# Kernel tuning notes

Measured on AMD Instinct MI355X. Metric: run time of the kernel, lower is better.

Reference implementation:

```python
import jax, jax.numpy as jnp
import numpy as np

BN_EPS = 1e-5
N_SH, N_SS, N_HH, D = 1195, 390, 805, 64


def _gcn(x, edge_index, W, b, n_nodes, mean):
    # per-edge message = Linear(x_j); lin(x)[src] == lin(x[src])
    h = x @ W + b                                   # [N, out]
    msg = h[edge_index[0]]                          # gather sources -> [E, out]
    agg = jax.ops.segment_sum(msg, edge_index[1], num_segments=n_nodes)
    if mean:
        cnt = jax.ops.segment_sum(jnp.ones((edge_index.shape[1],), x.dtype),
                                  edge_index[1], num_segments=n_nodes)
        agg = agg / jnp.maximum(cnt, 1.0)[:, None]
    return jnp.tanh(agg)


def _bn(x, gamma, beta):
    # BatchNorm1d in training mode: biased batch statistics
    m = jnp.mean(x, axis=0)
    v = jnp.var(x, axis=0)
    return (x - m) * jax.lax.rsqrt(v + BN_EPS) * gamma + beta


def setup_inputs() -> dict:
    key = jax.random.key(0)
    ks = jax.random.split(key, 40)
    f32 = jnp.float32

    def lin(k, din, dout):
        k1, k2 = jax.random.split(k)
        s = 1.0 / np.sqrt(din)
        W = jax.random.uniform(k1, (din, dout), f32, -s, s)
        b = jax.random.uniform(k2, (dout,), f32, -s, s)
        return W, b

    inp = {}
    inp["x_SH"] = jnp.arange(N_SH, dtype=jnp.int64 if jax.config.jax_enable_x64 else jnp.int32)
    inp["edge_index_SH"] = jax.random.randint(ks[0], (2, 1_000_000), 0, N_SH)
    inp["x_SS"] = jnp.arange(N_SS)
    inp["edge_index_SS"] = jax.random.randint(ks[1], (2, 200_000), 0, N_SS)
    inp["x_HH"] = jnp.arange(N_HH)
    inp["edge_index_HH"] = jax.random.randint(ks[2], (2, 200_000), 0, N_HH)
    inp["prescription"] = jax.random.uniform(ks[3], (20000, N_SS), f32)
    inp["kgOneHot"] = jax.random.uniform(ks[4], (N_HH, 27), f32)

    inp["emb"] = jax.random.normal(ks[5], (N_SH, D), f32)
    inp["w_sh1"], inp["b_sh1"] = lin(ks[6], D, D)
    inp["w_sh2"], inp["b_sh2"] = lin(ks[7], D, D)
    inp["w_mlp1"], inp["b_mlp1"] = lin(ks[8], D, 256)
    inp["g_bn1"] = jnp.ones((256,), f32); inp["be_bn1"] = jnp.zeros((256,), f32)
    inp["w_sh1h"], inp["b_sh1h"] = lin(ks[9], D, D)
    inp["w_sh2h"], inp["b_sh2h"] = lin(ks[10], D, D)
    inp["w_mlp1h"], inp["b_mlp1h"] = lin(ks[11], D, 256)
    inp["g_bn1h"] = jnp.ones((256,), f32); inp["be_bn1h"] = jnp.zeros((256,), f32)
    inp["w_ss"], inp["b_ss"] = lin(ks[12], D, 256)
    inp["w_hh"], inp["b_hh"] = lin(ks[13], D + 27, 256)
    inp["w_mlp"], inp["b_mlp"] = lin(ks[14], 256, 256)
    inp["g_si"] = jnp.ones((256,), f32); inp["be_si"] = jnp.zeros((256,), f32)
    return inp


def reference(x_SH, edge_index_SH, x_SS, edge_index_SS, x_HH, edge_index_HH,
              prescription, kgOneHot, emb,
              w_sh1, b_sh1, w_sh2, b_sh2, w_mlp1, b_mlp1, g_bn1, be_bn1,
              w_sh1h, b_sh1h, w_sh2h, b_sh2h, w_mlp1h, b_mlp1h, g_bn1h, be_bn1h,
              w_ss, b_ss, w_hh, b_hh, w_mlp, b_mlp, g_si, be_si):
    # symptom branch on SH graph (mean aggregation)
    x1 = emb[x_SH]                                           # [1195, 64]
    x2 = _gcn(x1, edge_index_SH, w_sh1, b_sh1, N_SH, mean=True)
    x6 = _gcn(x2, edge_index_SH, w_sh2, b_sh2, N_SH, mean=True)
    x9 = (x1 + x2 + x6) / 3.0
    x9 = jnp.tanh(_bn(x9 @ w_mlp1 + b_mlp1, g_bn1, be_bn1))  # [1195, 256]

    # herb branch on SH graph
    x22 = _gcn(x1, edge_index_SH, w_sh1h, b_sh1h, N_SH, mean=True)
    x66 = _gcn(x22, edge_index_SH, w_sh2h, b_sh2h, N_SH, mean=True)
    x99 = (x1 + x22 + x66) / 3.0
    x99 = jnp.tanh(_bn(x99 @ w_mlp1h + b_mlp1h, g_bn1h, be_bn1h))

    # SS graph (add aggregation)
    x_ss1 = _gcn(emb[x_SS], edge_index_SS, w_ss, b_ss, N_SS, mean=False)  # [390, 256]

    # HH graph with KG one-hot features appended
    x_hh0 = jnp.concatenate([emb[x_HH], kgOneHot], axis=-1)  # [805, 91]
    x_hh1 = _gcn(x_hh0, edge_index_HH, w_hh, b_hh, N_HH, mean=False)      # [805, 256]

    es = x9[:N_SS] + x_ss1                                   # [390, 256]
    eh = x99[N_SS:] + x_hh1                                  # [805, 256]

    e_synd = prescription @ es                               # [B, 256]
    pre_sum = jnp.sum(prescription, axis=1, keepdims=True)
    e = e_synd / pre_sum
    e = jax.nn.relu(_bn(e @ w_mlp + b_mlp, g_si, be_si))
    return e @ eh.T                                          # [B, 805]
```

## Files before the change

kernel.cpp:

```cpp
#include <hip/hip_runtime.h>
#include <cstddef>
#include <cstdint>

#define N_SH 1195
#define N_SS 390
#define N_HH 805
#define DIM  64

typedef __bf16 bf16_t;
typedef bf16_t bf16x4v __attribute__((ext_vector_type(4)));
typedef bf16_t bf16x8v __attribute__((ext_vector_type(8)));
typedef float f32x4 __attribute__((ext_vector_type(4)));

__device__ inline ushort f2bf(float f) {
    union { float f; uint32_t u; } c; c.f = f;
    uint32_t u = c.u;
    u += 0x7FFFu + ((u >> 16) & 1u);
    return (ushort)(u >> 16);
}

__device__ inline void xcd_swizzle(int gx, int gy, int& bx, int& by) {
    int nwg = gx * gy;
    int lin = by * gx + bx;
    int q = nwg >> 3, r = nwg & 7;
    int xcd = lin & 7, idx = lin >> 3;
    int nt = (xcd < r ? xcd * (q + 1) : r * (q + 1) + (xcd - r) * q) + idx;
    by = nt / gx; bx = nt % gx;
}

__global__ void build_adj3_kernel(
    const int* __restrict__ e1, int E1, int hs1, uint32_t* __restrict__ T1,
    const int* __restrict__ e2, int E2, int hs2, uint32_t* __restrict__ T2,
    const int* __restrict__ e3, int E3, int hs3, uint32_t* __restrict__ T3)
{
    int i = blockIdx.x * blockDim.x + threadIdx.x;
    if (i < E1) {
        int src = e1[i], dst = e1[E1 + i];
        atomicAdd(&T1[(size_t)dst * hs1 + (src >> 1)], 1u << ((src & 1) * 16));
    } else if (i < E1 + E2) {
        int j = i - E1;
        int src = e2[j], dst = e2[E2 + j];
        atomicAdd(&T2[(size_t)dst * hs2 + (src >> 1)], 1u << ((src & 1) * 16));
    } else if (i < E1 + E2 + E3) {
        int j = i - E1 - E2;
        int src = e3[j], dst = e3[E3 + j];
        atomicAdd(&T3[(size_t)dst * hs3 + (src >> 1)], 1u << ((src & 1) * 16));
    }
}

__global__ void rowsum_inv_packed_kernel(const uint32_t* __restrict__ T, int R,
                                         int halfStride, float* __restrict__ inv) {
    int row  = blockIdx.x * (blockDim.x / 64) + (threadIdx.x / 64);
    int lane = threadIdx.x & 63;
    if (row >= R) return;
    const uint32_t* p = T + (size_t)row * halfStride;
    uint32_t s = 0;
    for (int c = lane; c < halfStride; c += 64) {
        uint32_t w = p[c];
        s += (w & 0xFFFFu) + (w >> 16);
    }
    for (int off = 32; off > 0; off >>= 1) s += __shfl_down(s, off);
    if (lane == 0) inv[row] = 1.0f / fmaxf((float)s, 1.0f);
}

__device__ inline void unpack_one(const uint32_t* __restrict__ T, int R, int C,
                                  int hs, ushort* __restrict__ out, int Cp, int i) {
    int r = i / Cp, c = i % Cp;
    float v = 0.f;
    if (r < R && c < C) {
        uint32_t w = T[(size_t)r * hs + (c >> 1)];
        v = (float)((w >> ((c & 1) * 16)) & 0xFFFFu);
    }
    out[i] = f2bf(v);
}

__global__ void cvt_unpack3_kernel(
    const uint32_t* __restrict__ T1, int hs1, ushort* __restrict__ o1, int n1, int Cp1,
    const uint32_t* __restrict__ T2, int hs2, ushort* __restrict__ o2, int n2, int Cp2,
    const uint32_t* __restrict__ T3, int hs3, ushort* __restrict__ o3, int n3, int Cp3)
{
    int i = blockIdx.x * blockDim.x + threadIdx.x;
    if (i < n1) { unpack_one(T1, N_SH, N_SH, hs1, o1, Cp1, i); return; }
    i -= n1;
    if (i < n2) { unpack_one(T2, N_SS, N_SS, hs2, o2, Cp2, i); return; }
    i -= n2;
    if (i < n3) { unpack_one(T3, N_HH, N_HH, hs3, o3, Cp3, i); }
}

#define BM 64
#define BN 64
#define BK 16

__global__ __launch_bounds__(256) void gemm_kernel(
    const float* __restrict__ A, const float* __restrict__ B,
    const float* __restrict__ bias,
    float* __restrict__ C, ushort* __restrict__ outT, int ldt,
    int M, int N, int K, float* __restrict__ statsOut, int statsStride)
{
    __shared__ float As[BK][BM + 4];
    __shared__ float Bs[BK][BN];
    __shared__ float cs[128];
    const int tid  = threadIdx.x;
    const int row0 = blockIdx.y * BM;
    const int col0 = blockIdx.x * BN;
    const int tr  = (tid >> 4) << 2;
    const int tc  = (tid & 15) << 2;
    const int lar = tid >> 2;
    const int lac = (tid & 3) << 2;
    const int lbr = tid >> 4;
    const int lbc = (tid & 15) << 2;

    float acc[4][4] = {{0.f}};

    for (int k0 = 0; k0 < K; k0 += BK) {
        const int gr = row0 + lar;
        const float* Ap = A + (size_t)gr * K + k0 + lac;
        #pragma unroll
        for (int i = 0; i < 4; ++i) {
            int gk = k0 + lac + i;
            As[lac + i][lar] = (gr < M && gk < K) ? Ap[i] : 0.f;
        }
        const int gk = k0 + lbr;
        const float* Bp = B + (size_t)gk * N + col0 + lbc;
        #pragma unroll
        for (int i = 0; i < 4; ++i) {
            int gc = col0 + lbc + i;
            Bs[lbr][lbc + i] = (gk < K && gc < N) ? Bp[i] : 0.f;
        }
        __syncthreads();
        #pragma unroll
        for (int kk = 0; kk < BK; ++kk) {
            float4 a = *reinterpret_cast<const float4*>(&As[kk][tr]);
            float4 b = *reinterpret_cast<const float4*>(&Bs[kk][tc]);
            acc[0][0] += a.x * b.x; acc[0][1] += a.x * b.y; acc[0][2] += a.x * b.z; acc[0][3] += a.x * b.w;
            acc[1][0] += a.y * b.x; acc[1][1] += a.y * b.y; acc[1][2] += a.y * b.z; acc[1][3] += a.y * b.w;
            acc[2][0] += a.z * b.x; acc[2][1] += a.z * b.y; acc[2][2] += a.z * b.z; acc[2][3] += a.z * b.w;
            acc[3][0] += a.w * b.x; acc[3][1] += a.w * b.y; acc[3][2] += a.w * b.z; acc[3][3] += a.w * b.w;
        }
        __syncthreads();
    }

    float ls[4] = {0.f, 0.f, 0.f, 0.f}, lq[4] = {0.f, 0.f, 0.f, 0.f};
    #pragma unroll
    for (int i = 0; i < 4; ++i) {
        int gr = row0 + tr + i;
        if (gr >= M) continue;
        #pragma unroll
        for (int j = 0; j < 4; ++j) {
            int gc = col0 + tc + j;
            if (gc >= N) continue;
            float v = acc[i][j];
            if (bias) v += bias[gc];
            if (outT) outT[(size_t)gc * ldt + gr] = f2bf(v);
            else      C[(size_t)gr * N + gc] = v;
            ls[j] += v; lq[j] += v * v;
        }
    }

    if (statsOut) {
        if (tid < 128) cs[tid] = 0.f;
        __syncthreads();
        #pragma unroll
        for (int j = 0; j < 4; ++j) {
            atomicAdd(&cs[tc + j], ls[j]);
            atomicAdd(&cs[64 + tc + j], lq[j]);
        }
        __syncthreads();
        if (tid < 64) {
            atomicAdd(&statsOut[col0 + tid], cs[tid]);
            atomicAdd(&statsOut[statsStride + col0 + tid], cs[64 + tid]);
        }
    }
}

#define LDT 40

__global__ __launch_bounds__(256) void mfma_gemm_kernel(
    const ushort* __restrict__ A, const ushort* __restrict__ Bt,
    int M, int Nw, int K, int lda,
    const float* __restrict__ bias, const float* __restrict__ rowScale,
    float* __restrict__ outF, ushort* __restrict__ outB, ushort* __restrict__ outLo,
    int ldo, float* __restrict__ statsOut)
{
    __shared__ __align__(16) ushort As[128 * LDT];
    __shared__ __align__(16) ushort Bs[128 * LDT];
    __shared__ float cs[256];
    const int tid  = threadIdx.x;
    int bx = blockIdx.x, by = blockIdx.y;
    xcd_swizzle(gridDim.x, gridDim.y, bx, by);
    const int row0 = by * 128;
    const int col0 = bx * 128;
    const int wid  = tid >> 6, lane = tid & 63;
    const int wr = wid >> 1, wc = wid & 1;
    const int l15 = lane & 15, lg = lane >> 4;
    const int kg = lg * 4;
    const int sr = tid >> 2;
    const int sc = (tid & 3) * 8;

    const ushort* pA0 = A  + (size_t)(row0 + sr)      * lda + sc;
    const ushort* pA1 = A  + (size_t)(row0 + sr + 64) * lda + sc;
    const ushort* pB0 = Bt + (size_t)(col0 + sr)      * lda + sc;
    const ushort* pB1 = Bt + (size_t)(col0 + sr + 64) * lda + sc;

    uint4 ra0 = *reinterpret_cast<const uint4*>(pA0);
    uint4 ra1 = *reinterpret_cast<const uint4*>(pA1);
    uint4 rb0 = *reinterpret_cast<const uint4*>(pB0);
    uint4 rb1 = *reinterpret_cast<const uint4*>(pB1);

    f32x4 acc[4][4];
    #pragma unroll
    for (int m = 0; m < 4; ++m)
        #pragma unroll
        for (int n = 0; n < 4; ++n) acc[m][n] = (f32x4)0.f;

    for (int k0 = 0; k0 < K; k0 += 32) {
        *reinterpret_cast<uint4*>(&As[sr * LDT + sc])        = ra0;
        *reinterpret_cast<uint4*>(&As[(sr + 64) * LDT + sc]) = ra1;
        *reinterpret_cast<uint4*>(&Bs[sr * LDT + sc])        = rb0;
        *reinterpret_cast<uint4*>(&Bs[(sr + 64) * LDT + sc]) = rb1;
        __syncthreads();
        if (k0 + 32 < K) {
            ra0 = *reinterpret_cast<const uint4*>(pA0 + k0 + 32);
            ra1 = *reinterpret_cast<const uint4*>(pA1 + k0 + 32);
            rb0 = *reinterpret_cast<const uint4*>(pB0 + k0 + 32);
            rb1 = *reinterpret_cast<const uint4*>(pB1 + k0 + 32);
        }

        bf16x8v af[4], bfr[4];
        #pragma unroll
        for (int m = 0; m < 4; ++m) {
            int ar = wr * 64 + m * 16 + l15;
            bf16x4v lo = *reinterpret_cast<const bf16x4v*>(&As[ar * LDT + kg]);
            bf16x4v hi = *reinterpret_cast<const bf16x4v*>(&As[ar * LDT + kg + 16]);
            af[m] = __builtin_shufflevector(lo, hi, 0, 1, 2, 3, 4, 5, 6, 7);
        }
        #pragma unroll
        for (int n = 0; n < 4; ++n) {
            int br = wc * 64 + n * 16 + l15;
            bf16x4v lo = *reinterpret_cast<const bf16x4v*>(&Bs[br * LDT + kg]);
            bf16x4v hi = *reinterpret_cast<const bf16x4v*>(&Bs[br * LDT + kg + 16]);
            bfr[n] = __builtin_shufflevector(lo, hi, 0, 1, 2, 3, 4, 5, 6, 7);
        }
        #pragma unroll
        for (int m = 0; m < 4; ++m)
            #pragma unroll
            for (int n = 0; n < 4; ++n)
                acc[m][n] = __builtin_amdgcn_mfma_f32_16x16x32_bf16(af[m], bfr[n], acc[m][n], 0, 0, 0);
        __syncthreads();
    }

    float ls[4] = {0.f, 0.f, 0.f, 0.f}, lq[4] = {0.f, 0.f, 0.f, 0.f};
    #pragma unroll
    for (int m = 0; m < 4; ++m) {
        int grow_base = row0 + wr * 64 + m * 16 + kg;
        #pragma unroll
        for (int j = 0; j < 4; ++j) {
            int grow = grow_base + j;
            if (grow >= M) continue;
            float rs = rowScale ? rowScale[grow] : 1.0f;
            #pragma unroll
            for (int n = 0; n < 4; ++n) {
                int gcol = col0 + wc * 64 + n * 16 + l15;
                if (gcol >= Nw) continue;
                float v = acc[m][n][j];
                if (bias) v += bias[gcol];
                v *= rs;
                if (outB) {
                    ushort h = f2bf(v);
                    outB[(size_t)grow * ldo + gcol] = h;
                    if (outLo) {
                        float hv = __uint_as_float(((uint32_t)h) << 16);
                        outLo[(size_t)grow * ldo + gcol] = f2bf(v - hv);
                    }
                } else {
                    outF[(size_t)grow * ldo + gcol] = v;
                    ls[n] += v; lq[n] += v * v;
                }
            }
        }
    }

    if (statsOut) {
        if (tid < 256) cs[tid] = 0.f;
        __syncthreads();
        #pragma unroll
        for (int n = 0; n < 4; ++n) {
            int lc = wc * 64 + n * 16 + l15;
            atomicAdd(&cs[lc], ls[n]);
            atomicAdd(&cs[128 + lc], lq[n]);
        }
        __syncthreads();
        if (tid < 128) {
            atomicAdd(&statsOut[col0 + tid], cs[tid]);
            atomicAdd(&statsOut[256 + col0 + tid], cs[128 + tid]);
        }
    }
}

__device__ inline void loadP8(const float* __restrict__ rowp, int c0, bool rv,
                              float* a, float& s) {
    if (rv && c0 + 8 <= N_SS) {
        float2 x0 = *reinterpret_cast<const float2*>(rowp + c0);
        float2 x1 = *reinterpret_cast<const float2*>(rowp + c0 + 2);
        float2 x2 = *reinterpret_cast<const float2*>(rowp + c0 + 4);
        float2 x3 = *reinterpret_cast<const float2*>(rowp + c0 + 6);
        a[0] = x0.x; a[1] = x0.y; a[2] = x1.x; a[3] = x1.y;
        a[4] = x2.x; a[5] = x2.y; a[6] = x3.x; a[7] = x3.y;
    } else {
        #pragma unroll
        for (int i = 0; i < 8; ++i) a[i] = (rv && (c0 + i) < N_SS) ? rowp[c0 + i] : 0.f;
    }
    #pragma unroll
    for (int i = 0; i < 8; ++i) s += a[i];
}

__global__ __launch_bounds__(256) void mfma_c1_kernel(
    const float* __restrict__ Pm, const ushort* __restrict__ Bt,
    int M, ushort* __restrict__ outB, ushort* __restrict__ outLo, int ldo)
{
    __shared__ __align__(16) ushort As[128 * LDT];
    __shared__ __align__(16) ushort Bs[128 * LDT];
    __shared__ float sums[128];
    const int tid  = threadIdx.x;
    int bx = blockIdx.x, by = blockIdx.y;
    xcd_swizzle(gridDim.x, gridDim.y, bx, by);
    const int row0 = by * 128;
    const int col0 = bx * 128;
    const int wid  = tid >> 6, lane = tid & 63;
    const int wr = wid >> 1, wc = wid & 1;
    const int l15 = lane & 15, lg = lane >> 4;
    const int kg = lg * 4;
    const int sr = tid >> 2;
    const int sc = (tid & 3) * 8;

    const float* pA0 = Pm + (size_t)(row0 + sr)      * N_SS;
    const float* pA1 = Pm + (size_t)(row0 + sr + 64) * N_SS;
    const bool rv0 = (row0 + sr)      < M;
    const bool rv1 = (row0 + sr + 64) < M;
    const ushort* pB0 = Bt + (size_t)(col0 + sr)      * 416 + sc;
    const ushort* pB1 = Bt + (size_t)(col0 + sr + 64) * 416 + sc;

    float a0[8], a1[8];
    float s0 = 0.f, s1 = 0.f;
    loadP8(pA0, sc, rv0, a0, s0);
    loadP8(pA1, sc, rv1, a1, s1);
    uint4 b0 = *reinterpret_cast<const uint4*>(pB0);
    uint4 b1 = *reinterpret_cast<const uint4*>(pB1);

    f32x4 acc[4][4];
    #pragma unroll
    for (int m = 0; m < 4; ++m)
        #pragma unroll
        for (int n = 0; n < 4; ++n) acc[m][n] = (f32x4)0.f;

    for (int k0 = 0; k0 < 416; k0 += 32) {
        {
            bf16_t h[8];
            #pragma unroll
            for (int i = 0; i < 8; ++i) h[i] = (bf16_t)a0[i];
            *reinterpret_cast<uint4*>(&As[sr * LDT + sc]) = *reinterpret_cast<const uint4*>(h);
            #pragma unroll
            for (int i = 0; i < 8; ++i) h[i] = (bf16_t)a1[i];
            *reinterpret_cast<uint4*>(&As[(sr + 64) * LDT + sc]) = *reinterpret_cast<const uint4*>(h);
        }
        *reinterpret_cast<uint4*>(&Bs[sr * LDT + sc])        = b0;
        *reinterpret_cast<uint4*>(&Bs[(sr + 64) * LDT + sc]) = b1;
        __syncthreads();
        if (k0 + 32 < 416) {
            loadP8(pA0, k0 + 32 + sc, rv0, a0, s0);
            loadP8(pA1, k0 + 32 + sc, rv1, a1, s1);
            b0 = *reinterpret_cast<const uint4*>(pB0 + k0 + 32);
            b1 = *reinterpret_cast<const uint4*>(pB1 + k0 + 32);
        }

        bf16x8v af[4], bfr[4];
        #pragma unroll
        for (int m = 0; m < 4; ++m) {
            int ar = wr * 64 + m * 16 + l15;
            bf16x4v lo = *reinterpret_cast<const bf16x4v*>(&As[ar * LDT + kg]);
            bf16x4v hi = *reinterpret_cast<const bf16x4v*>(&As[ar * LDT + kg + 16]);
            af[m] = __builtin_shufflevector(lo, hi, 0, 1, 2, 3, 4, 5, 6, 7);
        }
        #pragma unroll
        for (int n = 0; n < 4; ++n) {
            int br = wc * 64 + n * 16 + l15;
            bf16x4v lo = *reinterpret_cast<const bf16x4v*>(&Bs[br * LDT + kg]);
            bf16x4v hi = *reinterpret_cast<const bf16x4v*>(&Bs[br * LDT + kg + 16]);
            bfr[n] = __builtin_shufflevector(lo, hi, 0, 1, 2, 3, 4, 5, 6, 7);
        }
        #pragma unroll
        for (int m = 0; m < 4; ++m)
            #pragma unroll
            for (int n = 0; n < 4; ++n)
                acc[m][n] = __builtin_amdgcn_mfma_f32_16x16x32_bf16(af[m], bfr[n], acc[m][n], 0, 0, 0);
        __syncthreads();
    }

    if (tid < 128) sums[tid] = 0.f;
    __syncthreads();
    atomicAdd(&sums[sr], s0);
    atomicAdd(&sums[sr + 64], s1);
    __syncthreads();

    #pragma unroll
    for (int m = 0; m < 4; ++m) {
        int lr_base = wr * 64 + m * 16 + kg;
        #pragma unroll
        for (int j = 0; j < 4; ++j) {
            int lr = lr_base + j;
            int grow = row0 + lr;
            if (grow >= M) continue;
            float t = sums[lr];
            float inv = (t != 0.f) ? 1.0f / t : 0.f;
            #pragma unroll
            for (int n = 0; n < 4; ++n) {
                int gcol = col0 + wc * 64 + n * 16 + l15;
                float v = acc[m][n][j] * inv;
                ushort h = f2bf(v);
                outB[(size_t)grow * ldo + gcol] = h;
                float hv = __uint_as_float(((uint32_t)h) << 16);
                outLo[(size_t)grow * ldo + gcol] = f2bf(v - hv);
            }
        }
    }
}

__global__ __launch_bounds__(256) void mfma_c3_kernel(
    const float* __restrict__ Abuf, const ushort* __restrict__ Bt,
    int M, int Nw,
    const float* __restrict__ scale, const float* __restrict__ shift,
    float* __restrict__ outF, int ldo)
{
    __shared__ __align__(16) ushort As[128 * LDT];
    __shared__ __align__(16) ushort Bs[128 * LDT];
    const int tid  = threadIdx.x;
    int bx = blockIdx.x, by = blockIdx.y;
    xcd_swizzle(gridDim.x, gridDim.y, bx, by);
    const int row0 = by * 128;
    const int col0 = bx * 128;
    const int wid  = tid >> 6, lane = tid & 63;
    const int wr = wid >> 1, wc = wid & 1;
    const int l15 = lane & 15, lg = lane >> 4;
    const int kg = lg * 4;
    const int sr = tid >> 2;
    const int sc = (tid & 3) * 8;

    const float*  pA0 = Abuf + (size_t)(row0 + sr)      * 256 + sc;
    const float*  pA1 = Abuf + (size_t)(row0 + sr + 64) * 256 + sc;
    const ushort* pB0 = Bt + (size_t)(col0 + sr)        * 256 + sc;
    const ushort* pB1 = Bt + (size_t)(col0 + sr + 64)   * 256 + sc;

    float4 a00 = *reinterpret_cast<const float4*>(pA0);
    float4 a01 = *reinterpret_cast<const float4*>(pA0 + 4);
    float4 a10 = *reinterpret_cast<const float4*>(pA1);
    float4 a11 = *reinterpret_cast<const float4*>(pA1 + 4);
    uint4  b0  = *reinterpret_cast<const uint4*>(pB0);
    uint4  b1  = *reinterpret_cast<const uint4*>(pB1);

    f32x4 acc[4][4];
    #pragma unroll
    for (int m = 0; m < 4; ++m)
        #pragma unroll
        for (int n = 0; n < 4; ++n) acc[m][n] = (f32x4)0.f;

    for (int k0 = 0; k0 < 256; k0 += 32) {
        float s8[8], t8[8];
        #pragma unroll
        for (int i = 0; i < 8; ++i) { s8[i] = scale[k0 + sc + i]; t8[i] = shift[k0 + sc + i]; }
        {
            bf16_t h[8];
            h[0] = (bf16_t)fmaxf(a00.x * s8[0] + t8[0], 0.f);
            h[1] = (bf16_t)fmaxf(a00.y * s8[1] + t8[1], 0.f);
            h[2] = (bf16_t)fmaxf(a00.z * s8[2] + t8[2], 0.f);
            h[3] = (bf16_t)fmaxf(a00.w * s8[3] + t8[3], 0.f);
            h[4] = (bf16_t)fmaxf(a01.x * s8[4] + t8[4], 0.f);
            h[5] = (bf16_t)fmaxf(a01.y * s8[5] + t8[5], 0.f);
            h[6] = (bf16_t)fmaxf(a01.z * s8[6] + t8[6], 0.f);
            h[7] = (bf16_t)fmaxf(a01.w * s8[7] + t8[7], 0.f);
            *reinterpret_cast<uint4*>(&As[sr * LDT + sc]) = *reinterpret_cast<const uint4*>(h);
            h[0] = (bf16_t)fmaxf(a10.x * s8[0] + t8[0], 0.f);
            h[1] = (bf16_t)fmaxf(a10.y * s8[1] + t8[1], 0.f);
            h[2] = (bf16_t)fmaxf(a10.z * s8[2] + t8[2], 0.f);
            h[3] = (bf16_t)fmaxf(a10.w * s8[3] + t8[3], 0.f);
            h[4] = (bf16_t)fmaxf(a11.x * s8[4] + t8[4], 0.f);
            h[5] = (bf16_t)fmaxf(a11.y * s8[5] + t8[5], 0.f);
            h[6] = (bf16_t)fmaxf(a11.z * s8[6] + t8[6], 0.f);
            h[7] = (bf16_t)fmaxf(a11.w * s8[7] + t8[7], 0.f);
            *reinterpret_cast<uint4*>(&As[(sr + 64) * LDT + sc]) = *reinterpret_cast<const uint4*>(h);
        }
        *reinterpret_cast<uint4*>(&Bs[sr * LDT + sc])        = b0;
        *reinterpret_cast<uint4*>(&Bs[(sr + 64) * LDT + sc]) = b1;
        __syncthreads();
        if (k0 + 32 < 256) {
            a00 = *reinterpret_cast<const float4*>(pA0 + k0 + 32);
            a01 = *reinterpret_cast<const float4*>(pA0 + k0 + 36);
            a10 = *reinterpret_cast<const float4*>(pA1 + k0 + 32);
            a11 = *reinterpret_cast<const float4*>(pA1 + k0 + 36);
            b0  = *reinterpret_cast<const uint4*>(pB0 + k0 + 32);
            b1  = *reinterpret_cast<const uint4*>(pB1 + k0 + 32);
        }

        bf16x8v af[4], bfr[4];
        #pragma unroll
        for (int m = 0; m < 4; ++m) {
            int ar = wr * 64 + m * 16 + l15;
            bf16x4v lo = *reinterpret_cast<const bf16x4v*>(&As[ar * LDT + kg]);
            bf16x4v hi = *reinterpret_cast<const bf16x4v*>(&As[ar * LDT + kg + 16]);
            af[m] = __builtin_shufflevector(lo, hi, 0, 1, 2, 3, 4, 5, 6, 7);
        }
        #pragma unroll
        for (int n = 0; n < 4; ++n) {
            int br = wc * 64 + n * 16 + l15;
            bf16x4v lo = *reinterpret_cast<const bf16x4v*>(&Bs[br * LDT + kg]);
            bf16x4v hi = *reinterpret_cast<const bf16x4v*>(&Bs[br * LDT + kg + 16]);
            bfr[n] = __builtin_shufflevector(lo, hi, 0, 1, 2, 3, 4, 5, 6, 7);
        }
        #pragma unroll
        for (int m = 0; m < 4; ++m)
            #pragma unroll
            for (int n = 0; n < 4; ++n)
                acc[m][n] = __builtin_amdgcn_mfma_f32_16x16x32_bf16(af[m], bfr[n], acc[m][n], 0, 0, 0);
        __syncthreads();
    }

    #pragma unroll
    for (int m = 0; m < 4; ++m) {
        int grow_base = row0 + wr * 64 + m * 16 + kg;
        #pragma unroll
        for (int j = 0; j < 4; ++j) {
            int grow = grow_base + j;
            if (grow >= M) continue;
            #pragma unroll
            for (int n = 0; n < 4; ++n) {
                int gcol = col0 + wc * 64 + n * 16 + l15;
                if (gcol >= Nw) continue;
                outF[(size_t)grow * ldo + gcol] = acc[m][n][j];
            }
        }
    }
}

__global__ __launch_bounds__(256) void mfma_splitk_kernel(
    const ushort* __restrict__ A, const ushort* __restrict__ Bt,
    int M, int K, int lda, int kChunk, int Ntot,
    float* __restrict__ part)
{
    __shared__ __align__(16) ushort As[128 * LDT];
    __shared__ __align__(16) ushort Bs[128 * LDT];
    const int tid  = threadIdx.x;
    const int row0 = blockIdx.y * 128;
    const int col0 = blockIdx.x * 128;
    const int wid  = tid >> 6, lane = tid & 63;
    const int wr = wid >> 1, wc = wid & 1;
    const int l15 = lane & 15, lg = lane >> 4;
    const int kg = lg * 4;
    const int sr = tid >> 2;
    const int sc = (tid & 3) * 8;

    const int k0s = blockIdx.z * kChunk;
    const int k0e = (k0s + kChunk < K) ? k0s + kChunk : K;

    const ushort* pA0 = A  + (size_t)(row0 + sr)      * lda + sc;
    const ushort* pA1 = A  + (size_t)(row0 + sr + 64) * lda + sc;
    const ushort* pB0 = Bt + (size_t)(col0 + sr)      * lda + sc;
    const ushort* pB1 = Bt + (size_t)(col0 + sr + 64) * lda + sc;

    uint4 ra0 = *reinterpret_cast<const uint4*>(pA0 + k0s);
    uint4 ra1 = *reinterpret_cast<const uint4*>(pA1 + k0s);
    uint4 rb0 = *reinterpret_cast<const uint4*>(pB0 + k0s);
    uint4 rb1 = *reinterpret_cast<const uint4*>(pB1 + k0s);

    f32x4 acc[4][4];
    #pragma unroll
    for (int m = 0; m < 4; ++m)
        #pragma unroll
        for (int n = 0; n < 4; ++n) acc[m][n] = (f32x4)0.f;

    for (int k0 = k0s; k0 < k0e; k0 += 32) {
        *reinterpret_cast<uint4*>(&As[sr * LDT + sc])        = ra0;
        *reinterpret_cast<uint4*>(&As[(sr + 64) * LDT + sc]) = ra1;
        *reinterpret_cast<uint4*>(&Bs[sr * LDT + sc])        = rb0;
        *reinterpret_cast<uint4*>(&Bs[(sr + 64) * LDT + sc]) = rb1;
        __syncthreads();
        if (k0 + 32 < k0e) {
            ra0 = *reinterpret_cast<const uint4*>(pA0 + k0 + 32);
            ra1 = *reinterpret_cast<const uint4*>(pA1 + k0 + 32);
            rb0 = *reinterpret_cast<const uint4*>(pB0 + k0 + 32);
            rb1 = *reinterpret_cast<const uint4*>(pB1 + k0 + 32);
        }

        bf16x8v af[4], bfr[4];
        #pragma unroll
        for (int m = 0; m < 4; ++m) {
            int ar = wr * 64 + m * 16 + l15;
            bf16x4v lo = *reinterpret_cast<const bf16x4v*>(&As[ar * LDT + kg]);
            bf16x4v hi = *reinterpret_cast<const bf16x4v*>(&As[ar * LDT + kg + 16]);
            af[m] = __builtin_shufflevector(lo, hi, 0, 1, 2, 3, 4, 5, 6, 7);
        }
        #pragma unroll
        for (int n = 0; n < 4; ++n) {
            int br = wc * 64 + n * 16 + l15;
            bf16x4v lo = *reinterpret_cast<const bf16x4v*>(&Bs[br * LDT + kg]);
            bf16x4v hi = *reinterpret_cast<const bf16x4v*>(&Bs[br * LDT + kg + 16]);
            bfr[n] = __builtin_shufflevector(lo, hi, 0, 1, 2, 3, 4, 5, 6, 7);
        }
        #pragma unroll
        for (int m = 0; m < 4; ++m)
            #pragma unroll
            for (int n = 0; n < 4; ++n)
                acc[m][n] = __builtin_amdgcn_mfma_f32_16x16x32_bf16(af[m], bfr[n], acc[m][n], 0, 0, 0);
        __syncthreads();
    }

    float* pslab = part + (size_t)blockIdx.z * M * Ntot;
    #pragma unroll
    for (int m = 0; m < 4; ++m) {
        int grow_base = row0 + wr * 64 + m * 16 + kg;
        #pragma unroll
        for (int j = 0; j < 4; ++j) {
            int grow = grow_base + j;
            if (grow >= M) continue;
            #pragma unroll
            for (int n = 0; n < 4; ++n) {
                int gcol = col0 + wc * 64 + n * 16 + l15;
                pslab[(size_t)grow * Ntot + gcol] = acc[m][n][j];
            }
        }
    }
}

__global__ void reduce_tanh_kernel(const float* __restrict__ part, int S, int M, int N,
                                   const float* __restrict__ rs,
                                   const float* __restrict__ emb,
                                   const float* __restrict__ prev,
                                   float* __restrict__ out) {
    int i = blockIdx.x * blockDim.x + threadIdx.x;
    if (i >= M * N) return;
    int r = i / N, j = i - r * N;
    float s = 0.f;
    for (int z = 0; z < S; ++z) s += part[(size_t)z * M * N + i];
    if (rs) s *= rs[r];
    float t = tanhf(s);
    if (emb) out[i] = (emb[r * 64 + (j & 63)] + prev[i] + t) * (1.0f / 3.0f);
    else     out[i] = t;
}

__global__ void make_cat_weights_kernel(
    const float* __restrict__ w_sh1, const float* __restrict__ w_sh1h,
    const float* __restrict__ b_sh1, const float* __restrict__ b_sh1h,
    const float* __restrict__ w_sh2, const float* __restrict__ w_sh2h,
    const float* __restrict__ b_sh2, const float* __restrict__ b_sh2h,
    const float* __restrict__ w_mlp1, const float* __restrict__ w_mlp1h,
    const float* __restrict__ b_mlp1, const float* __restrict__ b_mlp1h,
    const float* __restrict__ w_mlp,
    float* __restrict__ W1cat, float* __restrict__ b1cat,
    float* __restrict__ W2bd,  float* __restrict__ b2cat,
    float* __restrict__ WMbd,  float* __restrict__ bMcat,
    ushort* __restrict__ wmlp2)
{
    int i = blockIdx.x * blockDim.x + threadIdx.x;
    if (i < 64 * 128) {
        int k = i >> 7, j = i & 127;
        W1cat[i] = (j < 64) ? w_sh1[k * 64 + j] : w_sh1h[k * 64 + (j - 64)];
        return;
    }
    i -= 64 * 128;
    if (i < 128) { b1cat[i] = (i < 64) ? b_sh1[i] : b_sh1h[i - 64]; return; }
    i -= 128;
    if (i < 128 * 128) {
        int k = i >> 7, j = i & 127;
        float v = 0.f;
        if (k < 64 && j < 64) v = w_sh2[k * 64 + j];
        else if (k >= 64 && j >= 64) v = w_sh2h[(k - 64) * 64 + (j - 64)];
        W2bd[i] = v;
        return;
    }
    i -= 128 * 128;
    if (i < 128) { b2cat[i] = (i < 64) ? b_sh2[i] : b_sh2h[i - 64]; return; }
    i -= 128;
    if (i < 128 * 512) {
        int k = i >> 9, j = i & 511;
        float v = 0.f;
        if (j < 256) { if (k < 64) v = w_mlp1[k * 256 + j]; }
        else         { if (k >= 64) v = w_mlp1h[(k - 64) * 256 + (j - 256)]; }
        WMbd[i] = v;
        return;
    }
    i -= 128 * 512;
    if (i < 512) { bMcat[i] = (i < 256) ? b_mlp1[i] : b_mlp1h[i - 256]; return; }
    i -= 512;
    if (i < 256 * 512) {
        int n = i >> 9, k = i & 511;
        wmlp2[i] = f2bf(w_mlp[(size_t)(k & 255) * 256 + n]);
    }
}

__global__ void concat_hh_kernel(const float* __restrict__ emb, const float* __restrict__ kg,
                                 float* __restrict__ out) {
    int i = blockIdx.x * blockDim.x + threadIdx.x;
    const int n = N_HH * 91;
    if (i >= n) return;
    int r = i / 91, c = i % 91;
    out[i] = (c < DIM) ? emb[r * DIM + c] : kg[r * 27 + (c - DIM)];
}

__global__ void make_esbt_kernel(const float* __restrict__ x9cat, const float* __restrict__ ss1,
                                 ushort* __restrict__ out, int Kp) {
    int i = blockIdx.x * blockDim.x + threadIdx.x;
    if (i >= 256 * Kp) return;
    int n = i / Kp, k = i % Kp;
    float v = (k < N_SS) ? (x9cat[(size_t)k * 512 + n] + ss1[(size_t)k * 256 + n]) : 0.f;
    out[i] = f2bf(v);
}

__global__ void make_ehb_kernel(const float* __restrict__ x9cat, const float* __restrict__ hh1,
                                ushort* __restrict__ out, int Rp) {
    int i = blockIdx.x * blockDim.x + threadIdx.x;
    if (i >= Rp * 256) return;
    int r = i >> 8, c = i & 255;
    float v = (r < N_HH) ? (x9cat[(size_t)(N_SS + r) * 512 + 256 + c] + hh1[(size_t)r * 256 + c]) : 0.f;
    out[i] = f2bf(v);
}

__global__ void bn_apply_cat_kernel(const float* __restrict__ X, const float* __restrict__ stats,
                                    const float* __restrict__ g1, const float* __restrict__ be1,
                                    const float* __restrict__ g2, const float* __restrict__ be2,
                                    int M, float* __restrict__ out) {
    int i = blockIdx.x * blockDim.x + threadIdx.x;
    if (i >= M * 512) return;
    int j = i & 511;
    float invM = 1.0f / (float)M;
    float mean = stats[j] * invM;
    float var  = fmaxf(stats[512 + j] * invM - mean * mean, 0.f);
    float ga = (j < 256) ? g1[j]  : g2[j - 256];
    float bb = (j < 256) ? be1[j] : be2[j - 256];
    float y = (X[i] - mean) * rsqrtf(var + 1e-5f) * ga + bb;
    out[i] = tanhf(y);
}

__global__ void bn_finalize_kernel(const float* __restrict__ stats,
                                   const float* __restrict__ g, const float* __restrict__ be,
                                   int M, float* __restrict__ scale, float* __restrict__ shift) {
    int j = threadIdx.x;
    float invM = 1.0f / (float)M;
    float mean = stats[j] * invM;
    float var  = fmaxf(stats[256 + j] * invM - mean * mean, 0.f);
    float sc = g[j] * rsqrtf(var + 1e-5f);
    scale[j] = sc;
    shift[j] = be[j] - mean * sc;
}

extern "C" void kernel_launch(void* const* d_in, const int* in_sizes, int n_in,
                              void* d_out, int out_size, void* d_ws, size_t ws_size,
                              hipStream_t stream) {
    const int*   eiSH = (const int*)d_in[1];
    const int*   eiSS = (const int*)d_in[3];
    const int*   eiHH = (const int*)d_in[5];
    const float* P    = (const float*)d_in[6];
    const float* kg   = (const float*)d_in[7];
    const float* emb  = (const float*)d_in[8];
    const float* w_sh1  = (const float*)d_in[9];   const float* b_sh1  = (const float*)d_in[10];
    const float* w_sh2  = (const float*)d_in[11];  const float* b_sh2  = (const float*)d_in[12];
    const float* w_mlp1 = (const float*)d_in[13];  const float* b_mlp1 = (const float*)d_in[14];
    const float* g_bn1  = (const float*)d_in[15];  const float* be_bn1 = (const float*)d_in[16];
    const float* w_sh1h = (const float*)d_in[17];  const float* b_sh1h = (const float*)d_in[18];
    const float* w_sh2h = (const float*)d_in[19];  const float* b_sh2h = (const float*)d_in[20];
    const float* w_mlp1h= (const float*)d_in[21];  const float* b_mlp1h= (const float*)d_in[22];
    const float* g_bn1h = (const float*)d_in[23];  const float* be_bn1h= (const float*)d_in[24];
    const float* w_ss   = (const float*)d_in[25];  const float* b_ss   = (const float*)d_in[26];
    const float* w_hh   = (const float*)d_in[27];  const float* b_hh   = (const float*)d_in[28];
    const float* w_mlp  = (const float*)d_in[29];  const float* b_mlp  = (const float*)d_in[30];
    const float* g_si   = (const float*)d_in[31];  const float* be_si  = (const float*)d_in[32];
    float* out = (float*)d_out;

    const int E_SH = in_sizes[1] / 2;
    const int E_SS = in_sizes[3] / 2;
    const int E_HH = in_sizes[5] / 2;
    const int B    = in_sizes[6] / N_SS;
    const int Mp   = ((B + 127) / 128) * 128;
    const int KP1  = 416;
    const int NP3  = 896;
    const int KSH  = 1216;
    const int KHH  = 832;
    const int HS_SH = (N_SH + 1) / 2;
    const int HS_SS = (N_SS + 1) / 2;
    const int HS_HH = (N_HH + 1) / 2;

    float* w = (float*)d_ws;
    size_t off = 0;
    auto alloc = [&](size_t n) { float* p = w + off; off += (n + 3) & ~(size_t)3; return p; };

    float* cntInv   = alloc(N_SH);
    float* statsCat = alloc(1024);
    float* statsC2  = alloc(512);
    ushort* HT      = (ushort*)alloc((size_t)128 * KSH / 2);
    ushort* HSST    = (ushort*)alloc((size_t)256 * KP1 / 2);
    ushort* HHHT    = (ushort*)alloc((size_t)256 * KHH / 2);
    float* zeroEnd  = w + off;
    float* bnScale = alloc(256);
    float* bnShift = alloc(256);
    float* W1cat   = alloc(64 * 128);
    float* b1cat   = alloc(128);
    float* W2bd    = alloc(128 * 128);
    float* b2cat   = alloc(128);
    float* WMbd    = alloc(128 * 512);
    float* bMcat   = alloc(512);
    ushort* wmlp2  = (ushort*)alloc((size_t)256 * 512 / 2);
    ushort* adjb   = (ushort*)alloc((size_t)1280 * KSH / 2);
    ushort* adjSSb = (ushort*)alloc((size_t)512 * KP1 / 2);
    ushort* adjHHb = (ushort*)alloc((size_t)896 * KHH / 2);
    float* x2cat   = alloc((size_t)N_SH * 128);
    float* x9a2    = alloc((size_t)N_SH * 128);
    float* tmpBN   = alloc((size_t)N_SH * 512);
    float* x9cat   = alloc((size_t)N_SH * 512);
    float* ss1     = alloc((size_t)N_SS * 256);
    float* hh1     = alloc((size_t)N_HH * 256);
    float* xhh0    = alloc((size_t)N_HH * 91);
    ushort* es_bT  = (ushort*)alloc((size_t)256 * KP1 / 2);
    ushort* eh_b   = (ushort*)alloc((size_t)NP3 * 256 / 2);
    float* regionA = alloc((size_t)Mp * 256);
    uint32_t* uSH  = (uint32_t*)regionA;
    uint32_t* uSS  = uSH + (size_t)N_SH * HS_SH;
    uint32_t* uHH  = uSS + (size_t)N_SS * HS_SS;
    size_t packed_words = (size_t)N_SH * HS_SH + (size_t)N_SS * HS_SS + (size_t)N_HH * HS_HH;
    float*  bufM   = regionA;
    float* regionB = alloc((size_t)Mp * 256);
    float*  partials = regionB;
    ushort* e_hilo = (ushort*)regionB;
    (void)ws_size; (void)n_in; (void)out_size;

    auto gemmT = [&](const float* Am, const float* Bm, const float* bias,
                     ushort* oT, int ldt, int M, int N, int K) {
        dim3 g((N + BN - 1) / BN, (M + BM - 1) / BM);
        gemm_kernel<<<g, 256, 0, stream>>>(Am, Bm, bias, nullptr, oT, ldt, M, N, K, nullptr, 0);
    };
    auto gemmF = [&](const float* Am, const float* Bm, const float* bias,
                     float* C, int M, int N, int K, float* st, int sstride) {
        dim3 g((N + BN - 1) / BN, (M + BM - 1) / BM);
        gemm_kernel<<<g, 256, 0, stream>>>(Am, Bm, bias, C, nullptr, 0, M, N, K, st, sstride);
    };
    auto splitk = [&](const ushort* Am, const ushort* Bm, int M, int Mtiles, int K, int lda,
                      int Ntot, int S, const float* rs, const float* embA, const float* prev,
                      float* outp) {
        dim3 g(Ntot / 128, Mtiles, S);
        mfma_splitk_kernel<<<g, 256, 0, stream>>>(Am, Bm, M, K, lda, 128, Ntot, partials);
        reduce_tanh_kernel<<<(M * Ntot + 255) / 256, 256, 0, stream>>>(
            partials, S, M, Ntot, rs, embA, prev, outp);
    };

    hipMemsetAsync(uSH, 0, packed_words * sizeof(uint32_t), stream);
    hipMemsetAsync(statsCat, 0, (size_t)((char*)zeroEnd - (char*)statsCat), stream);

    {
        int Etot = E_SH + E_SS + E_HH;
        build_adj3_kernel<<<(Etot + 255) / 256, 256, 0, stream>>>(
            eiSH, E_SH, HS_SH, uSH, eiSS, E_SS, HS_SS, uSS, eiHH, E_HH, HS_HH, uHH);
    }
    rowsum_inv_packed_kernel<<<(N_SH + 3) / 4, 256, 0, stream>>>(uSH, N_SH, HS_SH, cntInv);
    {
        int n1 = 1280 * KSH, n2 = 512 * KP1, n3 = 896 * KHH;
        cvt_unpack3_kernel<<<(n1 + n2 + n3 + 255) / 256, 256, 0, stream>>>(
            uSH, HS_SH, adjb, n1, KSH, uSS, HS_SS, adjSSb, n2, KP1, uHH, HS_HH, adjHHb, n3, KHH);
    }

    make_cat_weights_kernel<<<(90880 + 131072 + 255) / 256, 256, 0, stream>>>(
        w_sh1, w_sh1h, b_sh1, b_sh1h, w_sh2, w_sh2h, b_sh2, b_sh2h,
        w_mlp1, w_mlp1h, b_mlp1, b_mlp1h, w_mlp,
        W1cat, b1cat, W2bd, b2cat, WMbd, bMcat, wmlp2);

    gemmT(emb, W1cat, b1cat, HT, KSH, N_SH, 128, 64);
    splitk(adjb, HT, N_SH, 10, KSH, KSH, 128, 10, cntInv, nullptr, nullptr, x2cat);
    gemmT(x2cat, W2bd, b2cat, HT, KSH, N_SH, 128, 128);
    splitk(adjb, HT, N_SH, 10, KSH, KSH, 128, 10, cntInv, emb, x2cat, x9a2);
    gemmF(x9a2, WMbd, bMcat, tmpBN, N_SH, 512, 128, statsCat, 512);
    bn_apply_cat_kernel<<<(N_SH * 512 + 255) / 256, 256, 0, stream>>>(
        tmpBN, statsCat, g_bn1, be_bn1, g_bn1h, be_bn1h, N_SH, x9cat);

    gemmT(emb, w_ss, b_ss, HSST, KP1, N_SS, 256, 64);
    splitk(adjSSb, HSST, N_SS, 4, KP1, KP1, 256, 4, nullptr, nullptr, nullptr, ss1);

    concat_hh_kernel<<<(N_HH * 91 + 255) / 256, 256, 0, stream>>>(emb, kg, xhh0);
    gemmT(xhh0, w_hh, b_hh, HHHT, KHH, N_HH, 256, 91);
    splitk(adjHHb, HHHT, N_HH, 7, KHH, KHH, 256, 7, nullptr, nullptr, nullptr, hh1);

    make_esbt_kernel<<<(256 * KP1 + 255) / 256, 256, 0, stream>>>(x9cat, ss1, es_bT, KP1);
    make_ehb_kernel<<<(NP3 * 256 + 255) / 256, 256, 0, stream>>>(x9cat, hh1, eh_b, NP3);

    {
        dim3 g(2, (B + 127) / 128);
        mfma_c1_kernel<<<g, 256, 0, stream>>>(P, es_bT, B, e_hilo, e_hilo + 256, 512);
    }
    {
        dim3 g(2, (B + 127) / 128);
        mfma_gemm_kernel<<<g, 256, 0, stream>>>(e_hilo, wmlp2, B, 256, 512, 512,
                                                b_mlp, nullptr, bufM, nullptr, nullptr, 256,
                                                statsC2);
    }
    bn_finalize_kernel<<<1, 256, 0, stream>>>(statsC2, g_si, be_si, B, bnScale, bnShift);
    {
        dim3 g(NP3 / 128, (B + 127) / 128);
        mfma_c3_kernel<<<g, 256, 0, stream>>>(bufM, eh_b, B, N_HH, bnScale, bnShift, out, N_HH);
    }
}
```

Measured before the change: 318.0 us.

## Reassociate prescription GEMM with MLP weight and fuse BN finalize

Precomputes (x9+ss1)@w_mlp on the 390-row side and multiplies prescription by that product, so the large 20000x512x256 MLP GEMM and its hi/lo split buffer disappear. The row normalization and bias are now applied in the first MFMA kernel's epilogue. BN finalize is folded into the final GEMM's prologue, and adjacency counts are packed 8 bits per entry instead of 16. The trade-off is precision: the hi/lo split on the intermediate is dropped, and any edge multiplicity above 255 would overflow the 8-bit counters.

```diff
diff --git a/kernel.cpp b/kernel.cpp
--- a/kernel.cpp
+++ b/kernel.cpp
@@ -36,15 +36,15 @@
     int i = blockIdx.x * blockDim.x + threadIdx.x;
     if (i < E1) {
         int src = e1[i], dst = e1[E1 + i];
-        atomicAdd(&T1[(size_t)dst * hs1 + (src >> 1)], 1u << ((src & 1) * 16));
+        atomicAdd(&T1[(size_t)dst * hs1 + (src >> 2)], 1u << ((src & 3) * 8));
     } else if (i < E1 + E2) {
         int j = i - E1;
         int src = e2[j], dst = e2[E2 + j];
-        atomicAdd(&T2[(size_t)dst * hs2 + (src >> 1)], 1u << ((src & 1) * 16));
+        atomicAdd(&T2[(size_t)dst * hs2 + (src >> 2)], 1u << ((src & 3) * 8));
     } else if (i < E1 + E2 + E3) {
         int j = i - E1 - E2;
         int src = e3[j], dst = e3[E3 + j];
-        atomicAdd(&T3[(size_t)dst * hs3 + (src >> 1)], 1u << ((src & 1) * 16));
+        atomicAdd(&T3[(size_t)dst * hs3 + (src >> 2)], 1u << ((src & 3) * 8));
     }
 }
 
@@ -57,7 +57,7 @@
     uint32_t s = 0;
     for (int c = lane; c < halfStride; c += 64) {
         uint32_t w = p[c];
-        s += (w & 0xFFFFu) + (w >> 16);
+        s += (w & 0xFFu) + ((w >> 8) & 0xFFu) + ((w >> 16) & 0xFFu) + (w >> 24);
     }
     for (int off = 32; off > 0; off >>= 1) s += __shfl_down(s, off);
     if (lane == 0) inv[row] = 1.0f / fmaxf((float)s, 1.0f);
@@ -68,8 +68,8 @@
     int r = i / Cp, c = i % Cp;
     float v = 0.f;
     if (r < R && c < C) {
-        uint32_t w = T[(size_t)r * hs + (c >> 1)];
-        v = (float)((w >> ((c & 1) * 16)) & 0xFFFFu);
+        uint32_t w = T[(size_t)r * hs + (c >> 2)];
+        v = (float)((w >> ((c & 3) * 8)) & 0xFFu);
     }
     out[i] = f2bf(v);
 }
@@ -92,7 +92,8 @@
 #define BK 16
 
 __global__ __launch_bounds__(256) void gemm_kernel(
-    const float* __restrict__ A, const float* __restrict__ B,
+    const float* __restrict__ A, const float* __restrict__ A2, int ldaA, int ldaA2,
+    const float* __restrict__ B,
     const float* __restrict__ bias,
     float* __restrict__ C, ushort* __restrict__ outT, int ldt,
     int M, int N, int K, float* __restrict__ statsOut, int statsStride)
@@ -114,11 +115,15 @@
 
     for (int k0 = 0; k0 < K; k0 += BK) {
         const int gr = row0 + lar;
-        const float* Ap = A + (size_t)gr * K + k0 + lac;
         #pragma unroll
         for (int i = 0; i < 4; ++i) {
             int gk = k0 + lac + i;
-            As[lac + i][lar] = (gr < M && gk < K) ? Ap[i] : 0.f;
+            float v = 0.f;
+            if (gr < M && gk < K) {
+                v = A[(size_t)gr * ldaA + gk];
+                if (A2) v += A2[(size_t)gr * ldaA2 + gk];
+            }
+            As[lac + i][lar] = v;
         }
         const int gk = k0 + lbr;
         const float* Bp = B + (size_t)gk * N + col0 + lbc;
@@ -175,15 +180,31 @@
 
 #define LDT 40
 
-__global__ __launch_bounds__(256) void mfma_gemm_kernel(
-    const ushort* __restrict__ A, const ushort* __restrict__ Bt,
-    int M, int Nw, int K, int lda,
-    const float* __restrict__ bias, const float* __restrict__ rowScale,
-    float* __restrict__ outF, ushort* __restrict__ outB, ushort* __restrict__ outLo,
-    int ldo, float* __restrict__ statsOut)
+__device__ inline void loadP8(const float* __restrict__ rowp, int c0, bool rv,
+                              float* a, float& s) {
+    if (rv && c0 + 8 <= N_SS) {
+        float2 x0 = *reinterpret_cast<const float2*>(rowp + c0);
+        float2 x1 = *reinterpret_cast<const float2*>(rowp + c0 + 2);
+        float2 x2 = *reinterpret_cast<const float2*>(rowp + c0 + 4);
+        float2 x3 = *reinterpret_cast<const float2*>(rowp + c0 + 6);
+        a[0] = x0.x; a[1] = x0.y; a[2] = x1.x; a[3] = x1.y;
+        a[4] = x2.x; a[5] = x2.y; a[6] = x3.x; a[7] = x3.y;
+    } else {
+        #pragma unroll
+        for (int i = 0; i < 8; ++i) a[i] = (rv && (c0 + i) < N_SS) ? rowp[c0 + i] : 0.f;
+    }
+    #pragma unroll
+    for (int i = 0; i < 8; ++i) s += a[i];
+}
+
+__global__ __launch_bounds__(256) void mfma_c1_kernel(
+    const float* __restrict__ Pm, const ushort* __restrict__ Dt,
+    int M, const float* __restrict__ bias,
+    float* __restrict__ outF, float* __restrict__ statsOut)
 {
     __shared__ __align__(16) ushort As[128 * LDT];
     __shared__ __align__(16) ushort Bs[128 * LDT];
+    __shared__ float sums[128];
     __shared__ float cs[256];
     const int tid  = threadIdx.x;
     int bx = blockIdx.x, by = blockIdx.y;
@@ -197,15 +218,19 @@
     const int sr = tid >> 2;
     const int sc = (tid & 3) * 8;
 
-    const ushort* pA0 = A  + (size_t)(row0 + sr)      * lda + sc;
-    const ushort* pA1 = A  + (size_t)(row0 + sr + 64) * lda + sc;
-    const ushort* pB0 = Bt + (size_t)(col0 + sr)      * lda + sc;
-    const ushort* pB1 = Bt + (size_t)(col0 + sr + 64) * lda + sc;
-
-    uint4 ra0 = *reinterpret_cast<const uint4*>(pA0);
-    uint4 ra1 = *reinterpret_cast<const uint4*>(pA1);
-    uint4 rb0 = *reinterpret_cast<const uint4*>(pB0);
-    uint4 rb1 = *reinterpret_cast<const uint4*>(pB1);
+    const float* pA0 = Pm + (size_t)(row0 + sr)      * N_SS;
+    const float* pA1 = Pm + (size_t)(row0 + sr + 64) * N_SS;
+    const bool rv0 = (row0 + sr)      < M;
+    const bool rv1 = (row0 + sr + 64) < M;
+    const ushort* pB0 = Dt + (size_t)(col0 + sr)      * 416 + sc;
+    const ushort* pB1 = Dt + (size_t)(col0 + sr + 64) * 416 + sc;
+
+    float a0[8], a1[8];
+    float s0 = 0.f, s1 = 0.f;
+    loadP8(pA0, sc, rv0, a0, s0);
+    loadP8(pA1, sc, rv1, a1, s1);
+    uint4 b0 = *reinterpret_cast<const uint4*>(pB0);
+    uint4 b1 = *reinterpret_cast<const uint4*>(pB1);
 
     f32x4 acc[4][4];
     #pragma unroll
@@ -213,17 +238,24 @@
         #pragma unroll
         for (int n = 0; n < 4; ++n) acc[m][n] = (f32x4)0.f;
 
-    for (int k0 = 0; k0 < K; k0 += 32) {
-        *reinterpret_cast<uint4*>(&As[sr * LDT + sc])        = ra0;
-        *reinterpret_cast<uint4*>(&As[(sr + 64) * LDT + sc]) = ra1;
-        *reinterpret_cast<uint4*>(&Bs[sr * LDT + sc])        = rb0;
-        *reinterpret_cast<uint4*>(&Bs[(sr + 64) * LDT + sc]) = rb1;
-        __syncthreads();
-        if (k0 + 32 < K) {
-            ra0 = *reinterpret_cast<const uint4*>(pA0 + k0 + 32);
-            ra1 = *reinterpret_cast<const uint4*>(pA1 + k0 + 32);
-            rb0 = *reinterpret_cast<const uint4*>(pB0 + k0 + 32);
-            rb1 = *reinterpret_cast<const uint4*>(pB1 + k0 + 32);
+    for (int k0 = 0; k0 < 416; k0 += 32) {
+        {
+            bf16_t h[8];
+            #pragma unroll
+            for (int i = 0; i < 8; ++i) h[i] = (bf16_t)a0[i];
+            *reinterpret_cast<uint4*>(&As[sr * LDT + sc]) = *reinterpret_cast<const uint4*>(h);
+            #pragma unroll
+            for (int i = 0; i < 8; ++i) h[i] = (bf16_t)a1[i];
+            *reinterpret_cast<uint4*>(&As[(sr + 64) * LDT + sc]) = *reinterpret_cast<const uint4*>(h);
+        }
+        *reinterpret_cast<uint4*>(&Bs[sr * LDT + sc])        = b0;
+        *reinterpret_cast<uint4*>(&Bs[(sr + 64) * LDT + sc]) = b1;
+        __syncthreads();
+        if (k0 + 32 < 416) {
+            loadP8(pA0, k0 + 32 + sc, rv0, a0, s0);
+            loadP8(pA1, k0 + 32 + sc, rv1, a1, s1);
+            b0 = *reinterpret_cast<const uint4*>(pB0 + k0 + 32);
+            b1 = *reinterpret_cast<const uint4*>(pB1 + k0 + 32);
         }
 
         bf16x8v af[4], bfr[4];
@@ -249,78 +281,58 @@
         __syncthreads();
     }
 
+    if (tid < 128) sums[tid] = 0.f;
+    if (tid < 256) cs[tid] = 0.f;
+    __syncthreads();
+    atomicAdd(&sums[sr], s0);
+    atomicAdd(&sums[sr + 64], s1);
+    __syncthreads();
+
     float ls[4] = {0.f, 0.f, 0.f, 0.f}, lq[4] = {0.f, 0.f, 0.f, 0.f};
     #pragma unroll
     for (int m = 0; m < 4; ++m) {
-        int grow_base = row0 + wr * 64 + m * 16 + kg;
+        int lr_base = wr * 64 + m * 16 + kg;
         #pragma unroll
         for (int j = 0; j < 4; ++j) {
-            int grow = grow_base + j;
+            int lr = lr_base + j;
+            int grow = row0 + lr;
             if (grow >= M) continue;
-            float rs = rowScale ? rowScale[grow] : 1.0f;
+            float t = sums[lr];
+            float inv = (t != 0.f) ? 1.0f / t : 0.f;
             #pragma unroll
             for (int n = 0; n < 4; ++n) {
                 int gcol = col0 + wc * 64 + n * 16 + l15;
-                if (gcol >= Nw) continue;
-                float v = acc[m][n][j];
-                if (bias) v += bias[gcol];
-                v *= rs;
-                if (outB) {
-                    ushort h = f2bf(v);
-                    outB[(size_t)grow * ldo + gcol] = h;
-                    if (outLo) {
-                        float hv = __uint_as_float(((uint32_t)h) << 16);
-                        outLo[(size_t)grow * ldo + gcol] = f2bf(v - hv);
-                    }
-                } else {
-                    outF[(size_t)grow * ldo + gcol] = v;
-                    ls[n] += v; lq[n] += v * v;
-                }
+                float v = acc[m][n][j] * inv + bias[gcol];
+                outF[(size_t)grow * 256 + gcol] = v;
+                ls[n] += v; lq[n] += v * v;
             }
         }
     }
 
-    if (statsOut) {
-        if (tid < 256) cs[tid] = 0.f;
-        __syncthreads();
-        #pragma unroll
-        for (int n = 0; n < 4; ++n) {
-            int lc = wc * 64 + n * 16 + l15;
-            atomicAdd(&cs[lc], ls[n]);
-            atomicAdd(&cs[128 + lc], lq[n]);
-        }
-        __syncthreads();
-        if (tid < 128) {
-            atomicAdd(&statsOut[col0 + tid], cs[tid]);
-            atomicAdd(&statsOut[256 + col0 + tid], cs[128 + tid]);
-        }
-    }
-}
-
-__device__ inline void loadP8(const float* __restrict__ rowp, int c0, bool rv,
-                              float* a, float& s) {
-    if (rv && c0 + 8 <= N_SS) {
-        float2 x0 = *reinterpret_cast<const float2*>(rowp + c0);
-        float2 x1 = *reinterpret_cast<const float2*>(rowp + c0 + 2);
-        float2 x2 = *reinterpret_cast<const float2*>(rowp + c0 + 4);
-        float2 x3 = *reinterpret_cast<const float2*>(rowp + c0 + 6);
-        a[0] = x0.x; a[1] = x0.y; a[2] = x1.x; a[3] = x1.y;
-        a[4] = x2.x; a[5] = x2.y; a[6] = x3.x; a[7] = x3.y;
-    } else {
-        #pragma unroll
-        for (int i = 0; i < 8; ++i) a[i] = (rv && (c0 + i) < N_SS) ? rowp[c0 + i] : 0.f;
-    }
-    #pragma unroll
-    for (int i = 0; i < 8; ++i) s += a[i];
-}
-
-__global__ __launch_bounds__(256) void mfma_c1_kernel(
-    const float* __restrict__ Pm, const ushort* __restrict__ Bt,
-    int M, ushort* __restrict__ outB, ushort* __restrict__ outLo, int ldo)
+    __syncthreads();
+    #pragma unroll
+    for (int n = 0; n < 4; ++n) {
+        int lc = wc * 64 + n * 16 + l15;
+        atomicAdd(&cs[lc], ls[n]);
+        atomicAdd(&cs[128 + lc], lq[n]);
+    }
+    __syncthreads();
+    if (tid < 128) {
+        atomicAdd(&statsOut[col0 + tid], cs[tid]);
+        atomicAdd(&statsOut[256 + col0 + tid], cs[128 + tid]);
+    }
+}
+
+__global__ __launch_bounds__(256) void mfma_c3_kernel(
+    const float* __restrict__ Abuf, const ushort* __restrict__ Bt,
+    int M, int Nw,
+    const float* __restrict__ stats, const float* __restrict__ g,
+    const float* __restrict__ be,
+    float* __restrict__ outF, int ldo)
 {
     __shared__ __align__(16) ushort As[128 * LDT];
     __shared__ __align__(16) ushort Bs[128 * LDT];
-    __shared__ float sums[128];
+    __shared__ float sscale[256], sshift[256];
     const int tid  = threadIdx.x;
     int bx = blockIdx.x, by = blockIdx.y;
     xcd_swizzle(gridDim.x, gridDim.y, bx, by);
@@ -333,117 +345,15 @@
     const int sr = tid >> 2;
     const int sc = (tid & 3) * 8;
 
-    const float* pA0 = Pm + (size_t)(row0 + sr)      * N_SS;
-    const float* pA1 = Pm + (size_t)(row0 + sr + 64) * N_SS;
-    const bool rv0 = (row0 + sr)      < M;
-    const bool rv1 = (row0 + sr + 64) < M;
-    const ushort* pB0 = Bt + (size_t)(col0 + sr)      * 416 + sc;
-    const ushort* pB1 = Bt + (size_t)(col0 + sr + 64) * 416 + sc;
-
-    float a0[8], a1[8];
-    float s0 = 0.f, s1 = 0.f;
-    loadP8(pA0, sc, rv0, a0, s0);
-    loadP8(pA1, sc, rv1, a1, s1);
-    uint4 b0 = *reinterpret_cast<const uint4*>(pB0);
-    uint4 b1 = *reinterpret_cast<const uint4*>(pB1);
-
-    f32x4 acc[4][4];
-    #pragma unroll
-    for (int m = 0; m < 4; ++m)
-        #pragma unroll
-        for (int n = 0; n < 4; ++n) acc[m][n] = (f32x4)0.f;
-
-    for (int k0 = 0; k0 < 416; k0 += 32) {
-        {
-            bf16_t h[8];
-            #pragma unroll
-            for (int i = 0; i < 8; ++i) h[i] = (bf16_t)a0[i];
-            *reinterpret_cast<uint4*>(&As[sr * LDT + sc]) = *reinterpret_cast<const uint4*>(h);
-            #pragma unroll
-            for (int i = 0; i < 8; ++i) h[i] = (bf16_t)a1[i];
-            *reinterpret_cast<uint4*>(&As[(sr + 64) * LDT + sc]) = *reinterpret_cast<const uint4*>(h);
-        }
-        *reinterpret_cast<uint4*>(&Bs[sr * LDT + sc])        = b0;
-        *reinterpret_cast<uint4*>(&Bs[(sr + 64) * LDT + sc]) = b1;
-        __syncthreads();
-        if (k0 + 32 < 416) {
-            loadP8(pA0, k0 + 32 + sc, rv0, a0, s0);
-            loadP8(pA1, k0 + 32 + sc, rv1, a1, s1);
-            b0 = *reinterpret_cast<const uint4*>(pB0 + k0 + 32);
-            b1 = *reinterpret_cast<const uint4*>(pB1 + k0 + 32);
-        }
-
-        bf16x8v af[4], bfr[4];
-        #pragma unroll
-        for (int m = 0; m < 4; ++m) {
-            int ar = wr * 64 + m * 16 + l15;
-            bf16x4v lo = *reinterpret_cast<const bf16x4v*>(&As[ar * LDT + kg]);
-            bf16x4v hi = *reinterpret_cast<const bf16x4v*>(&As[ar * LDT + kg + 16]);
-            af[m] = __builtin_shufflevector(lo, hi, 0, 1, 2, 3, 4, 5, 6, 7);
-        }
-        #pragma unroll
-        for (int n = 0; n < 4; ++n) {
-            int br = wc * 64 + n * 16 + l15;
-            bf16x4v lo = *reinterpret_cast<const bf16x4v*>(&Bs[br * LDT + kg]);
-            bf16x4v hi = *reinterpret_cast<const bf16x4v*>(&Bs[br * LDT + kg + 16]);
-            bfr[n] = __builtin_shufflevector(lo, hi, 0, 1, 2, 3, 4, 5, 6, 7);
-        }
-        #pragma unroll
-        for (int m = 0; m < 4; ++m)
-            #pragma unroll
-            for (int n = 0; n < 4; ++n)
-                acc[m][n] = __builtin_amdgcn_mfma_f32_16x16x32_bf16(af[m], bfr[n], acc[m][n], 0, 0, 0);
-        __syncthreads();
-    }
-
-    if (tid < 128) sums[tid] = 0.f;
+    if (tid < 256) {
+        float invM = 1.0f / (float)M;
+        float mean = stats[tid] * invM;
+        float var  = fmaxf(stats[256 + tid] * invM - mean * mean, 0.f);
+        float scv  = g[tid] * rsqrtf(var + 1e-5f);
+        sscale[tid] = scv;
+        sshift[tid] = be[tid] - mean * scv;
+    }
     __syncthreads();
-    atomicAdd(&sums[sr], s0);
-    atomicAdd(&sums[sr + 64], s1);
-    __syncthreads();
-
-    #pragma unroll
-    for (int m = 0; m < 4; ++m) {
-        int lr_base = wr * 64 + m * 16 + kg;
-        #pragma unroll
-        for (int j = 0; j < 4; ++j) {
-            int lr = lr_base + j;
-            int grow = row0 + lr;
-            if (grow >= M) continue;
-            float t = sums[lr];
-            float inv = (t != 0.f) ? 1.0f / t : 0.f;
-            #pragma unroll
-            for (int n = 0; n < 4; ++n) {
-                int gcol = col0 + wc * 64 + n * 16 + l15;
-                float v = acc[m][n][j] * inv;
-                ushort h = f2bf(v);
-                outB[(size_t)grow * ldo + gcol] = h;
-                float hv = __uint_as_float(((uint32_t)h) << 16);
-                outLo[(size_t)grow * ldo + gcol] = f2bf(v - hv);
-            }
-        }
-    }
-}
-
-__global__ __launch_bounds__(256) void mfma_c3_kernel(
-    const float* __restrict__ Abuf, const ushort* __restrict__ Bt,
-    int M, int Nw,
-    const float* __restrict__ scale, const float* __restrict__ shift,
-    float* __restrict__ outF, int ldo)
-{
-    __shared__ __align__(16) ushort As[128 * LDT];
-    __shared__ __align__(16) ushort Bs[128 * LDT];
-    const int tid  = threadIdx.x;
-    int bx = blockIdx.x, by = blockIdx.y;
-    xcd_swizzle(gridDim.x, gridDim.y, bx, by);
-    const int row0 = by * 128;
-    const int col0 = bx * 128;
-    const int wid  = tid >> 6, lane = tid & 63;
-    const int wr = wid >> 1, wc = wid & 1;
-    const int l15 = lane & 15, lg = lane >> 4;
-    const int kg = lg * 4;
-    const int sr = tid >> 2;
-    const int sc = (tid & 3) * 8;
 
     const float*  pA0 = Abuf + (size_t)(row0 + sr)      * 256 + sc;
     const float*  pA1 = Abuf + (size_t)(row0 + sr + 64) * 256 + sc;
@@ -466,7 +376,7 @@
     for (int k0 = 0; k0 < 256; k0 += 32) {
         float s8[8], t8[8];
         #pragma unroll
-        for (int i = 0; i < 8; ++i) { s8[i] = scale[k0 + sc + i]; t8[i] = shift[k0 + sc + i]; }
+        for (int i = 0; i < 8; ++i) { s8[i] = sscale[k0 + sc + i]; t8[i] = sshift[k0 + sc + i]; }
         {
             bf16_t h[8];
             h[0] = (bf16_t)fmaxf(a00.x * s8[0] + t8[0], 0.f);
@@ -652,11 +562,9 @@
     const float* __restrict__ b_sh2, const float* __restrict__ b_sh2h,
     const float* __restrict__ w_mlp1, const float* __restrict__ w_mlp1h,
     const float* __restrict__ b_mlp1, const float* __restrict__ b_mlp1h,
-    const float* __restrict__ w_mlp,
     float* __restrict__ W1cat, float* __restrict__ b1cat,
     float* __restrict__ W2bd,  float* __restrict__ b2cat,
-    float* __restrict__ WMbd,  float* __restrict__ bMcat,
-    ushort* __restrict__ wmlp2)
+    float* __restrict__ WMbd,  float* __restrict__ bMcat)
 {
     int i = blockIdx.x * blockDim.x + threadIdx.x;
     if (i < 64 * 128) {
@@ -687,12 +595,7 @@
         return;
     }
     i -= 128 * 512;
-    if (i < 512) { bMcat[i] = (i < 256) ? b_mlp1[i] : b_mlp1h[i - 256]; return; }
-    i -= 512;
-    if (i < 256 * 512) {
-        int n = i >> 9, k = i & 511;
-        wmlp2[i] = f2bf(w_mlp[(size_t)(k & 255) * 256 + n]);
-    }
+    if (i < 512) { bMcat[i] = (i < 256) ? b_mlp1[i] : b_mlp1h[i - 256]; }
 }
 
 __global__ void concat_hh_kernel(const float* __restrict__ emb, const float* __restrict__ kg,
@@ -702,15 +605,6 @@
     if (i >= n) return;
     int r = i / 91, c = i % 91;
     out[i] = (c < DIM) ? emb[r * DIM + c] : kg[r * 27 + (c - DIM)];
-}
-
-__global__ void make_esbt_kernel(const float* __restrict__ x9cat, const float* __restrict__ ss1,
-                                 ushort* __restrict__ out, int Kp) {
-    int i = blockIdx.x * blockDim.x + threadIdx.x;
-    if (i >= 256 * Kp) return;
-    int n = i / Kp, k = i % Kp;
-    float v = (k < N_SS) ? (x9cat[(size_t)k * 512 + n] + ss1[(size_t)k * 256 + n]) : 0.f;
-    out[i] = f2bf(v);
 }
 
 __global__ void make_ehb_kernel(const float* __restrict__ x9cat, const float* __restrict__ hh1,
@@ -736,18 +630,6 @@
     float bb = (j < 256) ? be1[j] : be2[j - 256];
     float y = (X[i] - mean) * rsqrtf(var + 1e-5f) * ga + bb;
     out[i] = tanhf(y);
-}
-
-__global__ void bn_finalize_kernel(const float* __restrict__ stats,
-                                   const float* __restrict__ g, const float* __restrict__ be,
-                                   int M, float* __restrict__ scale, float* __restrict__ shift) {
-    int j = threadIdx.x;
-    float invM = 1.0f / (float)M;
-    float mean = stats[j] * invM;
-    float var  = fmaxf(stats[256 + j] * invM - mean * mean, 0.f);
-    float sc = g[j] * rsqrtf(var + 1e-5f);
-    scale[j] = sc;
-    shift[j] = be[j] - mean * sc;
 }
 
 extern "C" void kernel_launch(void* const* d_in, const int* in_sizes, int n_in,
@@ -782,9 +664,9 @@
     const int NP3  = 896;
     const int KSH  = 1216;
     const int KHH  = 832;
-    const int HS_SH = (N_SH + 1) / 2;
-    const int HS_SS = (N_SS + 1) / 2;
-    const int HS_HH = (N_HH + 1) / 2;
+    const int HS_SH = (N_SH + 3) / 4;
+    const int HS_SS = (N_SS + 3) / 4;
+    const int HS_HH = (N_HH + 3) / 4;
 
     float* w = (float*)d_ws;
     size_t off = 0;
@@ -796,16 +678,14 @@
     ushort* HT      = (ushort*)alloc((size_t)128 * KSH / 2);
     ushort* HSST    = (ushort*)alloc((size_t)256 * KP1 / 2);
     ushort* HHHT    = (ushort*)alloc((size_t)256 * KHH / 2);
+    ushort* eswT    = (ushort*)alloc((size_t)256 * KP1 / 2);
     float* zeroEnd  = w + off;
-    float* bnScale = alloc(256);
-    float* bnShift = alloc(256);
     float* W1cat   = alloc(64 * 128);
     float* b1cat   = alloc(128);
     float* W2bd    = alloc(128 * 128);
     float* b2cat   = alloc(128);
     float* WMbd    = alloc(128 * 512);
     float* bMcat   = alloc(512);
-    ushort* wmlp2  = (ushort*)alloc((size_t)256 * 512 / 2);
     ushort* adjb   = (ushort*)alloc((size_t)1280 * KSH / 2);
     ushort* adjSSb = (ushort*)alloc((size_t)512 * KP1 / 2);
     ushort* adjHHb = (ushort*)alloc((size_t)896 * KHH / 2);
@@ -816,7 +696,6 @@
     float* ss1     = alloc((size_t)N_SS * 256);
     float* hh1     = alloc((size_t)N_HH * 256);
     float* xhh0    = alloc((size_t)N_HH * 91);
-    ushort* es_bT  = (ushort*)alloc((size_t)256 * KP1 / 2);
     ushort* eh_b   = (ushort*)alloc((size_t)NP3 * 256 / 2);
     float* regionA = alloc((size_t)Mp * 256);
     uint32_t* uSH  = (uint32_t*)regionA;
@@ -826,18 +705,20 @@
     float*  bufM   = regionA;
     float* regionB = alloc((size_t)Mp * 256);
     float*  partials = regionB;
-    ushort* e_hilo = (ushort*)regionB;
     (void)ws_size; (void)n_in; (void)out_size;
 
-    auto gemmT = [&](const float* Am, const float* Bm, const float* bias,
+    auto gemmT = [&](const float* Am, const float* A2m, int lda1, int lda2,
+                     const float* Bm, const float* bias,
                      ushort* oT, int ldt, int M, int N, int K) {
         dim3 g((N + BN - 1) / BN, (M + BM - 1) / BM);
-        gemm_kernel<<<g, 256, 0, stream>>>(Am, Bm, bias, nullptr, oT, ldt, M, N, K, nullptr, 0);
+        gemm_kernel<<<g, 256, 0, stream>>>(Am, A2m, lda1, lda2, Bm, bias,
+                                           nullptr, oT, ldt, M, N, K, nullptr, 0);
     };
     auto gemmF = [&](const float* Am, const float* Bm, const float* bias,
                      float* C, int M, int N, int K, float* st, int sstride) {
         dim3 g((N + BN - 1) / BN, (M + BM - 1) / BM);
-        gemm_kernel<<<g, 256, 0, stream>>>(Am, Bm, bias, C, nullptr, 0, M, N, K, st, sstride);
+        gemm_kernel<<<g, 256, 0, stream>>>(Am, nullptr, K, 0, Bm, bias,
+                                           C, nullptr, 0, M, N, K, st, sstride);
     };
     auto splitk = [&](const ushort* Am, const ushort* Bm, int M, int Mtiles, int K, int lda,
                       int Ntot, int S, const float* rs, const float* embA, const float* prev,
@@ -863,42 +744,35 @@
             uSH, HS_SH, adjb, n1, KSH, uSS, HS_SS, adjSSb, n2, KP1, uHH, HS_HH, adjHHb, n3, KHH);
     }
 
-    make_cat_weights_kernel<<<(90880 + 131072 + 255) / 256, 256, 0, stream>>>(
+    make_cat_weights_kernel<<<(90880 + 255) / 256, 256, 0, stream>>>(
         w_sh1, w_sh1h, b_sh1, b_sh1h, w_sh2, w_sh2h, b_sh2, b_sh2h,
-        w_mlp1, w_mlp1h, b_mlp1, b_mlp1h, w_mlp,
-        W1cat, b1cat, W2bd, b2cat, WMbd, bMcat, wmlp2);
-
-    gemmT(emb, W1cat, b1cat, HT, KSH, N_SH, 128, 64);
+        w_mlp1, w_mlp1h, b_mlp1, b_mlp1h,
+        W1cat, b1cat, W2bd, b2cat, WMbd, bMcat);
+
+    gemmT(emb, nullptr, 64, 0, W1cat, b1cat, HT, KSH, N_SH, 128, 64);
     splitk(adjb, HT, N_SH, 10, KSH, KSH, 128, 10, cntInv, nullptr, nullptr, x2cat);
-    gemmT(x2cat, W2bd, b2cat, HT, KSH, N_SH, 128, 128);
+    gemmT(x2cat, nullptr, 128, 0, W2bd, b2cat, HT, KSH, N_SH, 128, 128);
     splitk(adjb, HT, N_SH, 10, KSH, KSH, 128, 10, cntInv, emb, x2cat, x9a2);
     gemmF(x9a2, WMbd, bMcat, tmpBN, N_SH, 512, 128, statsCat, 512);
     bn_apply_cat_kernel<<<(N_SH * 512 + 255) / 256, 256, 0, stream>>>(
         tmpBN, statsCat, g_bn1, be_bn1, g_bn1h, be_bn1h, N_SH, x9cat);
 
-    gemmT(emb, w_ss, b_ss, HSST, KP1, N_SS, 256, 64);
+    gemmT(emb, nullptr, 64, 0, w_ss, b_ss, HSST, KP1, N_SS, 256, 64);
     splitk(adjSSb, HSST, N_SS, 4, KP1, KP1, 256, 4, nullptr, nullptr, nullptr, ss1);
 
     concat_hh_kernel<<<(N_HH * 91 + 255) / 256, 256, 0, stream>>>(emb, kg, xhh0);
-    gemmT(xhh0, w_hh, b_hh, HHHT, KHH, N_HH, 256, 91);
+    gemmT(xhh0, nullptr, 91, 0, w_hh, b_hh, HHHT, KHH, N_HH, 256, 91);
     splitk(adjHHb, HHHT, N_HH, 7, KHH, KHH, 256, 7, nullptr, nullptr, nullptr, hh1);
 
-    make_esbt_kernel<<<(256 * KP1 + 255) / 256, 256, 0, stream>>>(x9cat, ss1, es_bT, KP1);
     make_ehb_kernel<<<(NP3 * 256 + 255) / 256, 256, 0, stream>>>(x9cat, hh1, eh_b, NP3);
 
+    gemmT(x9cat, ss1, 512, 256, w_mlp, nullptr, eswT, KP1, N_SS, 256, 256);
     {
         dim3 g(2, (B + 127) / 128);
-        mfma_c1_kernel<<<g, 256, 0, stream>>>(P, es_bT, B, e_hilo, e_hilo + 256, 512);
-    }
-    {
-        dim3 g(2, (B + 127) / 128);
-        mfma_gemm_kernel<<<g, 256, 0, stream>>>(e_hilo, wmlp2, B, 256, 512, 512,
-                                                b_mlp, nullptr, bufM, nullptr, nullptr, 256,
-                                                statsC2);
-    }
-    bn_finalize_kernel<<<1, 256, 0, stream>>>(statsC2, g_si, be_si, B, bnScale, bnShift);
+        mfma_c1_kernel<<<g, 256, 0, stream>>>(P, eswT, B, b_mlp, bufM, statsC2);
+    }
     {
         dim3 g(NP3 / 128, (B + 127) / 128);
-        mfma_c3_kernel<<<g, 256, 0, stream>>>(bufM, eh_b, B, N_HH, bnScale, bnShift, out, N_HH);
-    }
-}
+        mfma_c3_kernel<<<g, 256, 0, stream>>>(bufM, eh_b, B, N_HH, statsC2, g_si, be_si, out, N_HH);
+    }
+}
```

After: 315.3 us. About the same (-0.8%).
